# Kernel optimization log

Hardware: AMD Instinct MI355X
Metric: run time of the kernel (lower is better)

The kernel has to match this reference:

```python
import jax, jax.numpy as jnp
import numpy as np
from jax.scipy.linalg import cho_solve

N, D, T, K, P = 4000, 256, 52, 20, 100
EPS = 1e-8


def _make_kernel(length_scale):
    # RBF kernel over time grid with the same jitter-doubling rule as the torch code.
    t = np.arange(T, dtype=np.float32)
    sq = (t[None, :] - t[:, None]) ** 2
    Kmat = np.exp(-0.5 * sq / np.float32(length_scale) ** 2).astype(np.float32)
    jitter = 1e-4
    eye = np.eye(T, dtype=np.float32)
    while True:
        if np.linalg.cond(Kmat + jitter * eye) < 1e4:
            break
        jitter *= 2
        if jitter > 0.1:
            break
    return jnp.asarray(Kmat + jitter * eye)

K_LAMBDA = _make_kernel(T / 4)  # lambda GP kernel, shared across all k
K_PHI = _make_kernel(T / 3)     # phi GP kernel, shared across all k


def setup_inputs() -> dict:
    key = jax.random.key(0)
    ks = jax.random.split(key, 7)
    lambda_ = jax.random.normal(ks[0], (N, K, T), dtype=jnp.float32)
    phi = jax.random.normal(ks[1], (K, D, T), dtype=jnp.float32)
    gamma = 0.1 * jax.random.normal(ks[2], (P, K), dtype=jnp.float32)
    G = jax.random.normal(ks[3], (N, P), dtype=jnp.float32)
    Y = (jax.random.uniform(ks[4], (N, D, T)) < 0.05).astype(jnp.float32)
    logit_prev_t = jax.random.normal(ks[5], (D, T), dtype=jnp.float32) - 3.0
    event_times = jax.random.randint(ks[6], (N, D), 0, T)
    return dict(lambda_=lambda_, phi=phi, gamma=gamma, G=G, Y=Y,
                logit_prev_t=logit_prev_t, event_times=event_times)


def reference(lambda_, phi, gamma, G, Y, logit_prev_t, event_times):
    # --- forward: softmax over topics, sigmoid disease probs, mixture ---
    theta = jax.nn.softmax(lambda_, axis=1)          # [N,K,T]
    phi_prob = jax.nn.sigmoid(phi)                   # [K,D,T]
    pi = jnp.einsum('nkt,kdt->ndt', theta, phi_prob) # [N,D,T]
    pi = jnp.clip(pi, EPS, 1.0 - EPS)

    # --- survival data loss ---
    tgrid = jnp.arange(T)[None, None, :]             # [1,1,T]
    e = event_times[:, :, None]                      # [N,D,1]
    mask_before = (tgrid < e).astype(pi.dtype)
    mask_at = (tgrid == e).astype(pi.dtype)
    log_pi = jnp.log(pi)
    log_1mpi = jnp.log1p(-pi)
    loss_censored = -jnp.sum(log_1mpi * mask_before)
    loss_event = -jnp.sum(log_pi * mask_at * Y)
    loss_no_event = -jnp.sum(log_1mpi * mask_at * (1.0 - Y))
    data_loss = (loss_censored + loss_event + loss_no_event) / N

    # --- GP prior loss: batched cholesky solves replace per-sample loops ---
    L_lam = jnp.linalg.cholesky(K_LAMBDA)            # [T,T]
    L_phi = jnp.linalg.cholesky(K_PHI)               # [T,T]
    mean_lam = G @ gamma                             # [N,K]
    dev_lam = (lambda_ - mean_lam[:, :, None]).reshape(N * K, T)  # [N*K,T]
    v_lam = cho_solve((L_lam, True), dev_lam.T)      # [T,N*K]
    gp_lambda = 0.5 * jnp.sum(dev_lam.T * v_lam)
    dev_phi = (phi - logit_prev_t[None, :, :]).reshape(K * D, T)  # [K*D,T]
    v_phi = cho_solve((L_phi, True), dev_phi.T)      # [T,K*D]
    gp_phi = 0.5 * jnp.sum(dev_phi.T * v_phi)
    gp_loss = gp_lambda / N + gp_phi / D

    return data_loss + gp_loss
```

## Files before the change

kernel.cpp:

```cpp
#include <hip/hip_runtime.h>
#include <math.h>
#include <string.h>

#define Nn 4000
#define Dd 256
#define Tt 52
#define Kk 20
#define Pp 100
#define TC 13

#define GRID_GRAM 145
#define GRID_DATA 2000
#define GRID_MAIN (GRID_GRAM + GRID_DATA)

#define PB_PHIP 52
#define PB_MEAN 313
#define GRID_PREP (PB_PHIP + PB_MEAN)

#define OFF_W     0
#define OFF_GPART 5408
#define OFF_DLP   5556
#define OFF_CNT   7556
#define OFF_M     7560
#define OFF_PHIP  87560

#define GR_ROWS 64

__global__ __launch_bounds__(256) void prep_kernel(
    const float* __restrict__ phi, const float* __restrict__ gamma,
    const float* __restrict__ G, float* __restrict__ phip_t,
    float* __restrict__ M, unsigned int* __restrict__ cnt) {
    const int bx = blockIdx.x, tid = threadIdx.x;
    if (bx < PB_PHIP) {
        if (bx == 0 && tid == 0) *cnt = 0u;
        int gid = bx * 256 + tid;
        int d = gid / Tt, t = gid - d * Tt;
        float v[Kk];
#pragma unroll
        for (int k = 0; k < Kk; ++k) {
            float x = phi[k * (Dd * Tt) + gid];
            v[k] = 1.f / (1.f + __expf(-x));
        }
#pragma unroll
        for (int k = 0; k < Kk; ++k)
            phip_t[((size_t)t * Kk + k) * Dd + d] = v[k];
        return;
    }
    int gid = (bx - PB_PHIP) * 256 + tid;
    if (gid < Nn * Kk) {
        int n = gid / Kk, k = gid - n * Kk;
        float m = 0.f;
        for (int p = 0; p < Pp; ++p) m += G[n * Pp + p] * gamma[p * Kk + k];
        M[gid] = m;
    }
}

__global__ __launch_bounds__(256) void main_kernel(
    const float* __restrict__ lam, const float* __restrict__ phi,
    const float* __restrict__ logit_prev, const int* __restrict__ ev,
    const float* __restrict__ Y, const float* __restrict__ phip_t,
    const float* __restrict__ M, const float* __restrict__ W,
    float* __restrict__ ws, float* __restrict__ out,
    unsigned int* __restrict__ cnt) {
    __shared__ union SM {
        struct { float thS[TC][8][Kk]; float lamS[8][Kk][TC + 1]; } d;
        struct { float rows[GR_ROWS][56]; } g;
    } sm;
    __shared__ double redd[256];
    __shared__ float wsum[4];
    __shared__ int isLast;
    const int bx = blockIdx.x, tid = threadIdx.x;

    if (bx < GRID_GRAM) {
        const bool isPhi = (bx >= 125);
        const int ntile = isPhi ? 4 : 10;
        const int base = isPhi ? (bx - 125) * 256 : bx * 640;
        const int ta = tid % 13, tb = tid / 13;
        float acc[4][4] = {};
        for (int it = 0; it < ntile; ++it) {
            const int R0 = base + it * GR_ROWS;
            __syncthreads();
            for (int idx = tid; idx < GR_ROWS * Tt; idx += 256) {
                int r = idx / Tt, t = idx - r * Tt;
                int R = R0 + r;
                float v;
                if (isPhi) v = phi[R * Tt + t] - logit_prev[(R & (Dd - 1)) * Tt + t];
                else       v = lam[R * Tt + t] - M[R];
                sm.g.rows[r][t] = v;
            }
            __syncthreads();
            if (tb < 13) {
                for (int r = 0; r < GR_ROWS; ++r) {
                    float4 a = *(const float4*)&sm.g.rows[r][4 * ta];
                    float4 b = *(const float4*)&sm.g.rows[r][4 * tb];
                    float av[4] = {a.x, a.y, a.z, a.w};
                    float bv[4] = {b.x, b.y, b.z, b.w};
#pragma unroll
                    for (int i = 0; i < 4; ++i)
#pragma unroll
                        for (int j = 0; j < 4; ++j) acc[i][j] += av[i] * bv[j];
                }
            }
        }
        double s = 0.0;
        if (tb < 13) {
            const float* Wb = W + (isPhi ? 2704 : 0);
#pragma unroll
            for (int i = 0; i < 4; ++i)
#pragma unroll
                for (int j = 0; j < 4; ++j)
                    s += (double)acc[i][j] *
                         (double)Wb[(4 * ta + i) * Tt + 4 * tb + j];
        }
        redd[tid] = s;
        __syncthreads();
        for (int off = 128; off; off >>= 1) {
            if (tid < off) redd[tid] += redd[tid + off];
            __syncthreads();
        }
        if (tid == 0) {
            ws[OFF_GPART + bx] = (float)redd[0];
            __threadfence();
            unsigned prev = atomicAdd(cnt, 1u);
            isLast = (prev == GRID_MAIN - 1) ? 1 : 0;
        }
    } else {
        const int bid = bx - GRID_GRAM;
        const int d = tid;
        const int ng = bid >> 2;
        const int chunk = bid & 3;
        const int t0 = chunk * TC;
        const int n0 = ng * 8;

        int e[8];
#pragma unroll
        for (int g = 0; g < 8; ++g) e[g] = ev[(n0 + g) * Dd + d];

        if (tid < 8 * Kk) {
            int n = tid / Kk, k = tid - n * Kk;
            const float* src = lam + ((size_t)(n0 + n) * Kk + k) * Tt + t0;
#pragma unroll
            for (int j = 0; j < TC; ++j) sm.d.lamS[n][k][j] = src[j];
        }
        __syncthreads();
        if (tid < 8 * TC) {
            int n = tid / TC, j = tid - n * TC;
            float v[Kk];
            float m = -1e30f;
#pragma unroll
            for (int k = 0; k < Kk; ++k) { v[k] = sm.d.lamS[n][k][j]; m = fmaxf(m, v[k]); }
            float s = 0.f;
#pragma unroll
            for (int k = 0; k < Kk; ++k) { v[k] = __expf(v[k] - m); s += v[k]; }
            float inv = 1.f / s;
#pragma unroll
            for (int k = 0; k < Kk; ++k) sm.d.thS[j][n][k] = v[k] * inv;
        }

        float Yv[8], acc[8], pie[8], prod[8];
#pragma unroll
        for (int g = 0; g < 8; ++g) {
            acc[g] = 0.f; prod[g] = 1.f; pie[g] = 0.5f; Yv[g] = 0.f;
            if ((unsigned)(e[g] - t0) < (unsigned)TC)
                Yv[g] = __builtin_nontemporal_load(
                    Y + (size_t)((n0 + g) * Dd + d) * Tt + e[g]);
        }
        __syncthreads();

        for (int j = 0; j < TC; ++j) {
            int t = t0 + j;
            float pv[Kk];
            const float* pt = phip_t + (size_t)t * (Kk * Dd) + d;
#pragma unroll
            for (int k = 0; k < Kk; ++k) pv[k] = pt[k * Dd];
#pragma unroll
            for (int g = 0; g < 8; ++g) {
                const float4* th = (const float4*)&sm.d.thS[j][g][0];
                float4 a0 = th[0], a1 = th[1], a2 = th[2], a3 = th[3], a4 = th[4];
                float pi = a0.x * pv[0] + a0.y * pv[1] + a0.z * pv[2] + a0.w * pv[3]
                         + a1.x * pv[4] + a1.y * pv[5] + a1.z * pv[6] + a1.w * pv[7]
                         + a2.x * pv[8] + a2.y * pv[9] + a2.z * pv[10] + a2.w * pv[11]
                         + a3.x * pv[12] + a3.y * pv[13] + a3.z * pv[14] + a3.w * pv[15]
                         + a4.x * pv[16] + a4.y * pv[17] + a4.z * pv[18] + a4.w * pv[19];
                pi = fminf(fmaxf(pi, 1e-8f), 1.0f - 1e-8f);
                prod[g] *= (t <= e[g]) ? (1.f - pi) : 1.f;
                pie[g] = (t == e[g]) ? pi : pie[g];
            }
            if ((j & 3) == 3 || j == TC - 1) {
#pragma unroll
                for (int g = 0; g < 8; ++g) { acc[g] += __logf(prod[g]); prod[g] = 1.f; }
            }
        }
        float tsum = 0.f;
#pragma unroll
        for (int g = 0; g < 8; ++g)
            tsum += acc[g] + Yv[g] * (__logf(pie[g]) - __logf(1.f - pie[g]));
        for (int off = 32; off; off >>= 1) tsum += __shfl_down(tsum, off, 64);
        if ((tid & 63) == 0) wsum[tid >> 6] = tsum;
        __syncthreads();
        if (tid == 0) {
            ws[OFF_DLP + bid] = -(wsum[0] + wsum[1] + wsum[2] + wsum[3]);
            __threadfence();
            unsigned prev = atomicAdd(cnt, 1u);
            isLast = (prev == GRID_MAIN - 1) ? 1 : 0;
        }
    }
    __syncthreads();
    if (!isLast) return;

    __threadfence();
    double s = 0.0;
    for (int i = tid; i < GRID_GRAM; i += 256) s += (double)ws[OFF_GPART + i];
    double dl = 0.0;
    for (int i = tid; i < GRID_DATA; i += 256) dl += (double)ws[OFF_DLP + i];
    s += dl / Nn;
    redd[tid] = s;
    __syncthreads();
    for (int off = 128; off; off >>= 1) {
        if (tid < off) redd[tid] += redd[tid + off];
        __syncthreads();
    }
    if (tid == 0) out[0] = (float)redd[0];
}


static void build_K_f(double ls_in, float Kf[52][52]) {
    float ls = (float)ls_in;
    float ls2 = ls * ls;
    for (int i = 0; i < 52; ++i)
        for (int j = 0; j < 52; ++j) {
            float sq = (float)((i - j) * (i - j));
            float arg = (-0.5f * sq) / ls2;
            Kf[i][j] = expf(arg);
        }
}

static void jacobi_eig(double a[52][52], double ev[52]) {
    const int n = 52;
    for (int sweep = 0; sweep < 100; ++sweep) {
        double off = 0;
        for (int p = 0; p < n - 1; ++p)
            for (int q = p + 1; q < n; ++q) off += a[p][q] * a[p][q];
        if (off < 1e-24) break;
        for (int p = 0; p < n - 1; ++p)
            for (int q = p + 1; q < n; ++q) {
                double apq = a[p][q];
                if (fabs(apq) < 1e-300) continue;
                double th = (a[q][q] - a[p][p]) / (2.0 * apq);
                double t = (th >= 0 ? 1.0 : -1.0) / (fabs(th) + sqrt(th * th + 1.0));
                double c = 1.0 / sqrt(t * t + 1.0), s = t * c;
                for (int i = 0; i < n; ++i) {
                    double aip = a[i][p], aiq = a[i][q];
                    a[i][p] = c * aip - s * aiq;
                    a[i][q] = s * aip + c * aiq;
                }
                for (int i = 0; i < n; ++i) {
                    double api = a[p][i], aqi = a[q][i];
                    a[p][i] = c * api - s * aqi;
                    a[q][i] = s * api + c * aqi;
                }
            }
    }
    for (int i = 0; i < n; ++i) ev[i] = a[i][i];
}

static void build_A(const float Kf[52][52], double jitter, double A[52][52]) {
    float jf = (float)jitter;
    for (int i = 0; i < 52; ++i)
        for (int j = 0; j < 52; ++j) A[i][j] = (double)Kf[i][j];
    for (int i = 0; i < 52; ++i) A[i][i] = (double)(float)(Kf[i][i] + jf);
}

static double cond_of(const float Kf[52][52], double jitter) {
    double A[52][52], ev[52];
    build_A(Kf, jitter, A);
    jacobi_eig(A, ev);
    double mx = 0.0, mn = 1e300;
    for (int i = 0; i < 52; ++i) {
        double a = fabs(ev[i]);
        if (a > mx) mx = a;
        if (a < mn) mn = a;
    }
    if (mn <= 0.0) return 1e300;
    return mx / mn;
}

static double find_jitter(const float Kf[52][52]) {
    double jitter = 1e-4;
    while (true) {
        if (cond_of(Kf, jitter) < 1e4) break;
        jitter *= 2.0;
        if (jitter > 0.1) break;
    }
    return jitter;
}

static void chol_inv_scaled(const float Kf[52][52], double jitter, double scale,
                            float* out) {
    const int n = 52;
    double A[52][52], L[52][52];
    build_A(Kf, jitter, A);
    memset(L, 0, sizeof(L));
    for (int j = 0; j < n; ++j) {
        double s = A[j][j];
        for (int k = 0; k < j; ++k) s -= L[j][k] * L[j][k];
        L[j][j] = sqrt(s);
        for (int i = j + 1; i < n; ++i) {
            double v = A[i][j];
            for (int k = 0; k < j; ++k) v -= L[i][k] * L[j][k];
            L[i][j] = v / L[j][j];
        }
    }
    for (int c = 0; c < n; ++c) {
        double y[52], x[52];
        for (int i = 0; i < n; ++i) {
            double v = (i == c) ? 1.0 : 0.0;
            for (int k = 0; k < i; ++k) v -= L[i][k] * y[k];
            y[i] = v / L[i][i];
        }
        for (int i = n - 1; i >= 0; --i) {
            double v = y[i];
            for (int k = i + 1; k < n; ++k) v -= L[k][i] * x[k];
            x[i] = v / L[i][i];
        }
        for (int i = 0; i < n; ++i) out[i * 52 + c] = (float)(x[i] * scale);
    }
}

struct KinvInit {
    float* w;
    KinvInit() {
        if (hipHostMalloc((void**)&w, 5408 * sizeof(float)) != hipSuccess)
            w = (float*)malloc(5408 * sizeof(float));
        float Kf[52][52];
        build_K_f(52.0 / 4.0, Kf);
        chol_inv_scaled(Kf, find_jitter(Kf), 0.5 / Nn, w);
        build_K_f(52.0 / 3.0, Kf);
        chol_inv_scaled(Kf, find_jitter(Kf), 0.5 / Dd, w + 2704);
    }
};
static KinvInit g_kinv;


extern "C" void kernel_launch(void* const* d_in, const int* in_sizes, int n_in,
                              void* d_out, int out_size, void* d_ws, size_t ws_size,
                              hipStream_t stream) {
    (void)in_sizes; (void)n_in; (void)out_size; (void)ws_size;
    const float* lam        = (const float*)d_in[0];
    const float* phi        = (const float*)d_in[1];
    const float* gamma      = (const float*)d_in[2];
    const float* G          = (const float*)d_in[3];
    const float* Y          = (const float*)d_in[4];
    const float* logit_prev = (const float*)d_in[5];
    const int*   ev         = (const int*)d_in[6];
    float* out = (float*)d_out;
    float* ws  = (float*)d_ws;

    hipMemcpyAsync(ws + OFF_W, g_kinv.w, 5408 * sizeof(float),
                   hipMemcpyHostToDevice, stream);

    prep_kernel<<<GRID_PREP, 256, 0, stream>>>(
        phi, gamma, G, ws + OFF_PHIP, ws + OFF_M,
        (unsigned int*)(ws + OFF_CNT));
    main_kernel<<<GRID_MAIN, 256, 0, stream>>>(
        lam, phi, logit_prev, ev, Y, ws + OFF_PHIP, ws + OFF_M, ws + OFF_W,
        ws, out, (unsigned int*)(ws + OFF_CNT));
}
```

Baseline: 436.4 us.

## Compute softmax per wavefront in registers and broadcast via readlane

Each wavefront now computes the topic softmax for its 8 samples × 13 timesteps directly in lane registers. It then broadcasts the needed theta values to every lane with readlane inside the mixture loop. This replaces the shared-memory staging and removes the two block-wide barriers in the data-loss path. The cost is that all four waves compute the softmax redundantly, the lambda loads become strided per lane, and each time step adds 160 readlane operations on top of the FMAs. The time loop is also no longer unrolled.

```diff
diff --git a/kernel.cpp b/kernel.cpp
--- a/kernel.cpp
+++ b/kernel.cpp
@@ -55,6 +55,38 @@
     }
 }
 
+#define RL(ARR, K, LN)                                                         \
+    __int_as_float(__builtin_amdgcn_readlane(__float_as_int(ARR[K]), (LN)))
+
+#define PIG(GG, ARR, LN) do {                                                  \
+    const int ln_ = (LN);                                                      \
+    float pi = RL(ARR,0,ln_)*pv[0] + RL(ARR,1,ln_)*pv[1]                       \
+             + RL(ARR,2,ln_)*pv[2] + RL(ARR,3,ln_)*pv[3]                       \
+             + RL(ARR,4,ln_)*pv[4] + RL(ARR,5,ln_)*pv[5]                       \
+             + RL(ARR,6,ln_)*pv[6] + RL(ARR,7,ln_)*pv[7]                       \
+             + RL(ARR,8,ln_)*pv[8] + RL(ARR,9,ln_)*pv[9]                       \
+             + RL(ARR,10,ln_)*pv[10] + RL(ARR,11,ln_)*pv[11]                   \
+             + RL(ARR,12,ln_)*pv[12] + RL(ARR,13,ln_)*pv[13]                   \
+             + RL(ARR,14,ln_)*pv[14] + RL(ARR,15,ln_)*pv[15]                   \
+             + RL(ARR,16,ln_)*pv[16] + RL(ARR,17,ln_)*pv[17]                   \
+             + RL(ARR,18,ln_)*pv[18] + RL(ARR,19,ln_)*pv[19];                  \
+    prod[GG] *= (t_ <= e[GG]) ? (1.f - pi) : 1.f;                              \
+    pie[GG] = (t_ == e[GG]) ? pi : pie[GG];                                    \
+} while (0)
+
+#define SOFTMAX_SET(TH, NBASE) do {                                            \
+    const float* la_ = lam + ((size_t)(NBASE) * Kk) * Tt + t0 + jl;            \
+    float m_ = -1e30f;                                                         \
+    _Pragma("unroll")                                                          \
+    for (int k = 0; k < Kk; ++k) { TH[k] = la_[k * Tt]; m_ = fmaxf(m_, TH[k]); } \
+    float s_ = 0.f;                                                            \
+    _Pragma("unroll")                                                          \
+    for (int k = 0; k < Kk; ++k) { TH[k] = __expf(TH[k] - m_); s_ += TH[k]; }  \
+    float inv_ = 1.f / s_;                                                     \
+    _Pragma("unroll")                                                          \
+    for (int k = 0; k < Kk; ++k) TH[k] *= inv_;                                \
+} while (0)
+
 __global__ __launch_bounds__(256) void main_kernel(
     const float* __restrict__ lam, const float* __restrict__ phi,
     const float* __restrict__ logit_prev, const int* __restrict__ ev,
@@ -62,10 +94,7 @@
     const float* __restrict__ M, const float* __restrict__ W,
     float* __restrict__ ws, float* __restrict__ out,
     unsigned int* __restrict__ cnt) {
-    __shared__ union SM {
-        struct { float thS[TC][8][Kk]; float lamS[8][Kk][TC + 1]; } d;
-        struct { float rows[GR_ROWS][56]; } g;
-    } sm;
+    __shared__ __align__(16) float rows[GR_ROWS][56];
     __shared__ double redd[256];
     __shared__ float wsum[4];
     __shared__ int isLast;
@@ -86,13 +115,13 @@
                 float v;
                 if (isPhi) v = phi[R * Tt + t] - logit_prev[(R & (Dd - 1)) * Tt + t];
                 else       v = lam[R * Tt + t] - M[R];
-                sm.g.rows[r][t] = v;
+                rows[r][t] = v;
             }
             __syncthreads();
             if (tb < 13) {
                 for (int r = 0; r < GR_ROWS; ++r) {
-                    float4 a = *(const float4*)&sm.g.rows[r][4 * ta];
-                    float4 b = *(const float4*)&sm.g.rows[r][4 * tb];
+                    float4 a = *(const float4*)&rows[r][4 * ta];
+                    float4 b = *(const float4*)&rows[r][4 * tb];
                     float av[4] = {a.x, a.y, a.z, a.w};
                     float bv[4] = {b.x, b.y, b.z, b.w};
 #pragma unroll
@@ -131,31 +160,18 @@
         const int chunk = bid & 3;
         const int t0 = chunk * TC;
         const int n0 = ng * 8;
+        const int lane = tid & 63;
+
+        int nl = lane / 13; if (nl > 3) nl = 3;
+        int jl = (lane < 52) ? lane - nl * 13 : 12;
 
         int e[8];
 #pragma unroll
         for (int g = 0; g < 8; ++g) e[g] = ev[(n0 + g) * Dd + d];
 
-        if (tid < 8 * Kk) {
-            int n = tid / Kk, k = tid - n * Kk;
-            const float* src = lam + ((size_t)(n0 + n) * Kk + k) * Tt + t0;
-#pragma unroll
-            for (int j = 0; j < TC; ++j) sm.d.lamS[n][k][j] = src[j];
-        }
-        __syncthreads();
-        if (tid < 8 * TC) {
-            int n = tid / TC, j = tid - n * TC;
-            float v[Kk];
-            float m = -1e30f;
-#pragma unroll
-            for (int k = 0; k < Kk; ++k) { v[k] = sm.d.lamS[n][k][j]; m = fmaxf(m, v[k]); }
-            float s = 0.f;
-#pragma unroll
-            for (int k = 0; k < Kk; ++k) { v[k] = __expf(v[k] - m); s += v[k]; }
-            float inv = 1.f / s;
-#pragma unroll
-            for (int k = 0; k < Kk; ++k) sm.d.thS[j][n][k] = v[k] * inv;
-        }
+        float thA[Kk], thB[Kk];
+        SOFTMAX_SET(thA, n0 + nl);
+        SOFTMAX_SET(thB, n0 + 4 + nl);
 
         float Yv[8], acc[8], pie[8], prod[8];
 #pragma unroll
@@ -165,32 +181,28 @@
                 Yv[g] = __builtin_nontemporal_load(
                     Y + (size_t)((n0 + g) * Dd + d) * Tt + e[g]);
         }
-        __syncthreads();
-
+
+#pragma unroll 1
         for (int j = 0; j < TC; ++j) {
-            int t = t0 + j;
+            const int t_ = t0 + j;
             float pv[Kk];
-            const float* pt = phip_t + (size_t)t * (Kk * Dd) + d;
-#pragma unroll
-            for (int k = 0; k < Kk; ++k) pv[k] = pt[k * Dd];
-#pragma unroll
-            for (int g = 0; g < 8; ++g) {
-                const float4* th = (const float4*)&sm.d.thS[j][g][0];
-                float4 a0 = th[0], a1 = th[1], a2 = th[2], a3 = th[3], a4 = th[4];
-                float pi = a0.x * pv[0] + a0.y * pv[1] + a0.z * pv[2] + a0.w * pv[3]
-                         + a1.x * pv[4] + a1.y * pv[5] + a1.z * pv[6] + a1.w * pv[7]
-                         + a2.x * pv[8] + a2.y * pv[9] + a2.z * pv[10] + a2.w * pv[11]
-                         + a3.x * pv[12] + a3.y * pv[13] + a3.z * pv[14] + a3.w * pv[15]
-                         + a4.x * pv[16] + a4.y * pv[17] + a4.z * pv[18] + a4.w * pv[19];
-                pi = fminf(fmaxf(pi, 1e-8f), 1.0f - 1e-8f);
-                prod[g] *= (t <= e[g]) ? (1.f - pi) : 1.f;
-                pie[g] = (t == e[g]) ? pi : pie[g];
-            }
-            if ((j & 3) == 3 || j == TC - 1) {
+            const float* pt_ = phip_t + (size_t)t_ * (Kk * Dd) + d;
+#pragma unroll
+            for (int k = 0; k < Kk; ++k) pv[k] = pt_[k * Dd];
+            PIG(0, thA, j);
+            PIG(1, thA, 13 + j);
+            PIG(2, thA, 26 + j);
+            PIG(3, thA, 39 + j);
+            PIG(4, thB, j);
+            PIG(5, thB, 13 + j);
+            PIG(6, thB, 26 + j);
+            PIG(7, thB, 39 + j);
+            if (((j & 3) == 3) || (j == TC - 1)) {
 #pragma unroll
                 for (int g = 0; g < 8; ++g) { acc[g] += __logf(prod[g]); prod[g] = 1.f; }
             }
         }
+
         float tsum = 0.f;
 #pragma unroll
         for (int g = 0; g < 8; ++g)
```

Result: slower. 458.5 us (+5.1%).

## Halve main kernel block size, giving each thread two disease columns

Applied to the files above, without the earlier changes.

The main kernel now launches 128 threads per block. Each data-loss thread handles two disease indices so the shared softmax theta values in LDS are reused across two dot products, and the Gram blocks give some threads a second 4x4 tile. The softmax now reads lambda directly from global memory instead of staging it through shared memory, which drops one barrier and the lamS buffer. The goal is more reuse and less LDS traffic per FLOP, at the cost of higher register pressure and lower thread-level parallelism per block.

```diff
diff --git a/kernel.cpp b/kernel.cpp
--- a/kernel.cpp
+++ b/kernel.cpp
@@ -55,18 +55,25 @@
     }
 }
 
-__global__ __launch_bounds__(256) void main_kernel(
+#define PICHAIN(PV)                                                            \
+    (a0.x*PV[0] + a0.y*PV[1] + a0.z*PV[2] + a0.w*PV[3]                         \
+   + a1.x*PV[4] + a1.y*PV[5] + a1.z*PV[6] + a1.w*PV[7]                         \
+   + a2.x*PV[8] + a2.y*PV[9] + a2.z*PV[10] + a2.w*PV[11]                       \
+   + a3.x*PV[12] + a3.y*PV[13] + a3.z*PV[14] + a3.w*PV[15]                     \
+   + a4.x*PV[16] + a4.y*PV[17] + a4.z*PV[18] + a4.w*PV[19])
+
+__global__ __launch_bounds__(128) void main_kernel(
     const float* __restrict__ lam, const float* __restrict__ phi,
     const float* __restrict__ logit_prev, const int* __restrict__ ev,
     const float* __restrict__ Y, const float* __restrict__ phip_t,
     const float* __restrict__ M, const float* __restrict__ W,
     float* __restrict__ ws, float* __restrict__ out,
     unsigned int* __restrict__ cnt) {
-    __shared__ union SM {
-        struct { float thS[TC][8][Kk]; float lamS[8][Kk][TC + 1]; } d;
-        struct { float rows[GR_ROWS][56]; } g;
+    __shared__ __align__(16) union SM {
+        float thS[TC][8][Kk];
+        float rows[GR_ROWS][56];
     } sm;
-    __shared__ double redd[256];
+    __shared__ double redd[128];
     __shared__ float wsum[4];
     __shared__ int isLast;
     const int bx = blockIdx.x, tid = threadIdx.x;
@@ -76,45 +83,60 @@
         const int ntile = isPhi ? 4 : 10;
         const int base = isPhi ? (bx - 125) * 256 : bx * 640;
         const int ta = tid % 13, tb = tid / 13;
-        float acc[4][4] = {};
+        const int ta2 = (tid + 128) % 13, tb2 = (tid + 128) / 13;
+        const bool hasB = (tid < 41);
+        float accA[4][4] = {}, accB[4][4] = {};
         for (int it = 0; it < ntile; ++it) {
             const int R0 = base + it * GR_ROWS;
             __syncthreads();
-            for (int idx = tid; idx < GR_ROWS * Tt; idx += 256) {
+            for (int idx = tid; idx < GR_ROWS * Tt; idx += 128) {
                 int r = idx / Tt, t = idx - r * Tt;
                 int R = R0 + r;
                 float v;
                 if (isPhi) v = phi[R * Tt + t] - logit_prev[(R & (Dd - 1)) * Tt + t];
                 else       v = lam[R * Tt + t] - M[R];
-                sm.g.rows[r][t] = v;
+                sm.rows[r][t] = v;
             }
             __syncthreads();
-            if (tb < 13) {
-                for (int r = 0; r < GR_ROWS; ++r) {
-                    float4 a = *(const float4*)&sm.g.rows[r][4 * ta];
-                    float4 b = *(const float4*)&sm.g.rows[r][4 * tb];
-                    float av[4] = {a.x, a.y, a.z, a.w};
-                    float bv[4] = {b.x, b.y, b.z, b.w};
+            for (int r = 0; r < GR_ROWS; ++r) {
+                float4 a = *(const float4*)&sm.rows[r][4 * ta];
+                float4 b = *(const float4*)&sm.rows[r][4 * tb];
+                float av[4] = {a.x, a.y, a.z, a.w};
+                float bv[4] = {b.x, b.y, b.z, b.w};
+#pragma unroll
+                for (int i = 0; i < 4; ++i)
+#pragma unroll
+                    for (int j = 0; j < 4; ++j) accA[i][j] += av[i] * bv[j];
+                if (hasB) {
+                    float4 a2 = *(const float4*)&sm.rows[r][4 * ta2];
+                    float4 b2 = *(const float4*)&sm.rows[r][4 * tb2];
+                    float av2[4] = {a2.x, a2.y, a2.z, a2.w};
+                    float bv2[4] = {b2.x, b2.y, b2.z, b2.w};
 #pragma unroll
                     for (int i = 0; i < 4; ++i)
 #pragma unroll
-                        for (int j = 0; j < 4; ++j) acc[i][j] += av[i] * bv[j];
+                        for (int j = 0; j < 4; ++j) accB[i][j] += av2[i] * bv2[j];
                 }
             }
         }
-        double s = 0.0;
-        if (tb < 13) {
-            const float* Wb = W + (isPhi ? 2704 : 0);
+        const float* Wb = W + (isPhi ? 2704 : 0);
+        double sA = 0.0, sB = 0.0;
+#pragma unroll
+        for (int i = 0; i < 4; ++i)
+#pragma unroll
+            for (int j = 0; j < 4; ++j)
+                sA += (double)accA[i][j] * (double)Wb[(4 * ta + i) * Tt + 4 * tb + j];
+        if (hasB) {
 #pragma unroll
             for (int i = 0; i < 4; ++i)
 #pragma unroll
                 for (int j = 0; j < 4; ++j)
-                    s += (double)acc[i][j] *
-                         (double)Wb[(4 * ta + i) * Tt + 4 * tb + j];
-        }
-        redd[tid] = s;
+                    sB += (double)accB[i][j] *
+                          (double)Wb[(4 * ta2 + i) * Tt + 4 * tb2 + j];
+        }
+        redd[tid] = sA + sB;
         __syncthreads();
-        for (int off = 128; off; off >>= 1) {
+        for (int off = 64; off; off >>= 1) {
             if (tid < off) redd[tid] += redd[tid + off];
             __syncthreads();
         }
@@ -126,77 +148,93 @@
         }
     } else {
         const int bid = bx - GRID_GRAM;
-        const int d = tid;
         const int ng = bid >> 2;
         const int chunk = bid & 3;
         const int t0 = chunk * TC;
         const int n0 = ng * 8;
-
-        int e[8];
-#pragma unroll
-        for (int g = 0; g < 8; ++g) e[g] = ev[(n0 + g) * Dd + d];
-
-        if (tid < 8 * Kk) {
-            int n = tid / Kk, k = tid - n * Kk;
-            const float* src = lam + ((size_t)(n0 + n) * Kk + k) * Tt + t0;
-#pragma unroll
-            for (int j = 0; j < TC; ++j) sm.d.lamS[n][k][j] = src[j];
-        }
-        __syncthreads();
+        const int d0 = tid, d1 = tid + 128;
+
         if (tid < 8 * TC) {
             int n = tid / TC, j = tid - n * TC;
+            const float* la = lam + ((size_t)(n0 + n) * Kk) * Tt + t0 + j;
             float v[Kk];
             float m = -1e30f;
 #pragma unroll
-            for (int k = 0; k < Kk; ++k) { v[k] = sm.d.lamS[n][k][j]; m = fmaxf(m, v[k]); }
+            for (int k = 0; k < Kk; ++k) { v[k] = la[k * Tt]; m = fmaxf(m, v[k]); }
             float s = 0.f;
 #pragma unroll
             for (int k = 0; k < Kk; ++k) { v[k] = __expf(v[k] - m); s += v[k]; }
             float inv = 1.f / s;
 #pragma unroll
-            for (int k = 0; k < Kk; ++k) sm.d.thS[j][n][k] = v[k] * inv;
-        }
-
-        float Yv[8], acc[8], pie[8], prod[8];
+            for (int k = 0; k < Kk; ++k) sm.thS[j][n][k] = v[k] * inv;
+        }
+
+        int e[16];
 #pragma unroll
         for (int g = 0; g < 8; ++g) {
+            e[g]     = ev[(n0 + g) * Dd + d0];
+            e[8 + g] = ev[(n0 + g) * Dd + d1];
+        }
+
+        float Yv[16], acc[16], pie[16], prod[16];
+#pragma unroll
+        for (int g = 0; g < 16; ++g) {
             acc[g] = 0.f; prod[g] = 1.f; pie[g] = 0.5f; Yv[g] = 0.f;
+        }
+#pragma unroll
+        for (int g = 0; g < 8; ++g) {
             if ((unsigned)(e[g] - t0) < (unsigned)TC)
                 Yv[g] = __builtin_nontemporal_load(
-                    Y + (size_t)((n0 + g) * Dd + d) * Tt + e[g]);
+                    Y + (size_t)((n0 + g) * Dd + d0) * Tt + e[g]);
+            if ((unsigned)(e[8 + g] - t0) < (unsigned)TC)
+                Yv[8 + g] = __builtin_nontemporal_load(
+                    Y + (size_t)((n0 + g) * Dd + d1) * Tt + e[8 + g]);
         }
         __syncthreads();
 
+#pragma unroll 1
         for (int j = 0; j < TC; ++j) {
-            int t = t0 + j;
-            float pv[Kk];
-            const float* pt = phip_t + (size_t)t * (Kk * Dd) + d;
-#pragma unroll
-            for (int k = 0; k < Kk; ++k) pv[k] = pt[k * Dd];
+            const int t_ = t0 + j;
+            float pv0[Kk], pv1[Kk];
+            const float* pt_ = phip_t + (size_t)t_ * (Kk * Dd);
+#pragma unroll
+            for (int k = 0; k < Kk; ++k) {
+                pv0[k] = pt_[k * Dd + d0];
+                pv1[k] = pt_[k * Dd + d1];
+            }
 #pragma unroll
             for (int g = 0; g < 8; ++g) {
-                const float4* th = (const float4*)&sm.d.thS[j][g][0];
+                const float4* th = (const float4*)&sm.thS[j][g][0];
                 float4 a0 = th[0], a1 = th[1], a2 = th[2], a3 = th[3], a4 = th[4];
-                float pi = a0.x * pv[0] + a0.y * pv[1] + a0.z * pv[2] + a0.w * pv[3]
-                         + a1.x * pv[4] + a1.y * pv[5] + a1.z * pv[6] + a1.w * pv[7]
-                         + a2.x * pv[8] + a2.y * pv[9] + a2.z * pv[10] + a2.w * pv[11]
-                         + a3.x * pv[12] + a3.y * pv[13] + a3.z * pv[14] + a3.w * pv[15]
-                         + a4.x * pv[16] + a4.y * pv[17] + a4.z * pv[18] + a4.w * pv[19];
-                pi = fminf(fmaxf(pi, 1e-8f), 1.0f - 1e-8f);
-                prod[g] *= (t <= e[g]) ? (1.f - pi) : 1.f;
-                pie[g] = (t == e[g]) ? pi : pie[g];
-            }
-            if ((j & 3) == 3 || j == TC - 1) {
-#pragma unroll
-                for (int g = 0; g < 8; ++g) { acc[g] += __logf(prod[g]); prod[g] = 1.f; }
-            }
-        }
-        float tsum = 0.f;
-#pragma unroll
-        for (int g = 0; g < 8; ++g)
-            tsum += acc[g] + Yv[g] * (__logf(pie[g]) - __logf(1.f - pie[g]));
-        for (int off = 32; off; off >>= 1) tsum += __shfl_down(tsum, off, 64);
-        if ((tid & 63) == 0) wsum[tid >> 6] = tsum;
+                float piA = PICHAIN(pv0);
+                float piB = PICHAIN(pv1);
+                prod[g]     *= (t_ <= e[g])     ? (1.f - piA) : 1.f;
+                pie[g]       = (t_ == e[g])     ? piA : pie[g];
+                prod[8 + g] *= (t_ <= e[8 + g]) ? (1.f - piB) : 1.f;
+                pie[8 + g]   = (t_ == e[8 + g]) ? piB : pie[8 + g];
+            }
+            if (((j & 3) == 3) || (j == TC - 1)) {
+#pragma unroll
+                for (int g = 0; g < 16; ++g) { acc[g] += __logf(prod[g]); prod[g] = 1.f; }
+            }
+        }
+
+        float tsumA = 0.f, tsumB = 0.f;
+#pragma unroll
+        for (int g = 0; g < 8; ++g) {
+            tsumA += acc[g] + Yv[g] * (__logf(pie[g]) - __logf(1.f - pie[g]));
+            tsumB += acc[8 + g] +
+                     Yv[8 + g] * (__logf(pie[8 + g]) - __logf(1.f - pie[8 + g]));
+        }
+        for (int off = 32; off; off >>= 1) {
+            tsumA += __shfl_down(tsumA, off, 64);
+            tsumB += __shfl_down(tsumB, off, 64);
+        }
+        if ((tid & 63) == 0) {
+            int w = tid >> 6;
+            wsum[w] = tsumA;
+            wsum[2 + w] = tsumB;
+        }
         __syncthreads();
         if (tid == 0) {
             ws[OFF_DLP + bid] = -(wsum[0] + wsum[1] + wsum[2] + wsum[3]);
@@ -209,14 +247,17 @@
     if (!isLast) return;
 
     __threadfence();
-    double s = 0.0;
-    for (int i = tid; i < GRID_GRAM; i += 256) s += (double)ws[OFF_GPART + i];
-    double dl = 0.0;
-    for (int i = tid; i < GRID_DATA; i += 256) dl += (double)ws[OFF_DLP + i];
-    s += dl / Nn;
-    redd[tid] = s;
+    double sA = 0.0, sB = 0.0;
+    for (int i = tid; i < GRID_GRAM; i += 256) sA += (double)ws[OFF_GPART + i];
+    for (int i = tid + 128; i < GRID_GRAM; i += 256) sB += (double)ws[OFF_GPART + i];
+    double dlA = 0.0, dlB = 0.0;
+    for (int i = tid; i < GRID_DATA; i += 256) dlA += (double)ws[OFF_DLP + i];
+    for (int i = tid + 128; i < GRID_DATA; i += 256) dlB += (double)ws[OFF_DLP + i];
+    sA += dlA / Nn;
+    sB += dlB / Nn;
+    redd[tid] = sA + sB;
     __syncthreads();
-    for (int off = 128; off; off >>= 1) {
+    for (int off = 64; off; off >>= 1) {
         if (tid < off) redd[tid] += redd[tid + off];
         __syncthreads();
     }
@@ -362,7 +403,7 @@
     prep_kernel<<<GRID_PREP, 256, 0, stream>>>(
         phi, gamma, G, ws + OFF_PHIP, ws + OFF_M,
         (unsigned int*)(ws + OFF_CNT));
-    main_kernel<<<GRID_MAIN, 256, 0, stream>>>(
+    main_kernel<<<GRID_MAIN, 128, 0, stream>>>(
         lam, phi, logit_prev, ev, Y, ws + OFF_PHIP, ws + OFF_M, ws + OFF_W,
         ws, out, (unsigned int*)(ws + OFF_CNT));
 }
```

New measurement: 424.6 us. 2.7% less time.
